# Optimization experiments

Measured on AMD Instinct MI355X. Metric: run time of the kernel, lower is better.

Reference implementation:

```python
import jax, jax.numpy as jnp
import numpy as np
from jax import lax

B, C_IN, L = 16, 2, 8192
D, H, NL = 256, 8, 4
DK = D // H
DFF = 2 * D
S = L // 8  # downsampled length = 1024
EPS = 1e-5


def _pe(seq, d):
    pos = jnp.arange(seq, dtype=jnp.float32)[:, None]
    div = jnp.exp(jnp.arange(0, d, 2, dtype=jnp.float32) * (-np.log(10000.0) / d))
    pe = jnp.zeros((seq, d), dtype=jnp.float32)
    pe = pe.at[:, 0::2].set(jnp.sin(pos * div))
    pe = pe.at[:, 1::2].set(jnp.cos(pos * div))
    return pe  # (seq, d)


def _layernorm(x, g, b):
    m = jnp.mean(x, axis=-1, keepdims=True)
    v = jnp.mean((x - m) ** 2, axis=-1, keepdims=True)
    return (x - m) * lax.rsqrt(v + EPS) * g + b


def setup_inputs() -> dict:
    key = jax.random.key(0)
    ks = jax.random.split(key, 20)
    sd = 0.02
    inp = {
        'x': jax.random.normal(ks[0], (B, C_IN, L), jnp.float32),
        'conv1_w': jax.random.normal(ks[1], (32, C_IN, 8), jnp.float32) * sd,
        'conv1_b': jnp.zeros((32,), jnp.float32),
        'conv2_w': jax.random.normal(ks[2], (D, 32, 4), jnp.float32) * sd,
        'conv2_b': jnp.zeros((D,), jnp.float32),
        'wq': jax.random.normal(ks[3], (NL, D, D), jnp.float32) * sd,
        'bq': jnp.zeros((NL, D), jnp.float32),
        'wk': jax.random.normal(ks[4], (NL, D, D), jnp.float32) * sd,
        'bk': jnp.zeros((NL, D), jnp.float32),
        'wv': jax.random.normal(ks[5], (NL, D, D), jnp.float32) * sd,
        'bv': jnp.zeros((NL, D), jnp.float32),
        'wo': jax.random.normal(ks[6], (NL, D, D), jnp.float32) * sd,
        'bo': jnp.zeros((NL, D), jnp.float32),
        'ln1_g': jnp.ones((NL, D), jnp.float32),
        'ln1_b': jnp.zeros((NL, D), jnp.float32),
        'ff_w1': jax.random.normal(ks[7], (NL, D, DFF), jnp.float32) * sd,
        'ff_b1': jnp.zeros((NL, DFF), jnp.float32),
        'ff_w2': jax.random.normal(ks[8], (NL, DFF, D), jnp.float32) * sd,
        'ff_b2': jnp.zeros((NL, D), jnp.float32),
        'ln2_g': jnp.ones((NL, D), jnp.float32),
        'ln2_b': jnp.zeros((NL, D), jnp.float32),
        'cls_w1': jax.random.normal(ks[9], (D, D // 2), jnp.float32) * sd,
        'cls_b1': jnp.zeros((D // 2,), jnp.float32),
        'cls_w2': jax.random.normal(ks[10], (D // 2, 1), jnp.float32) * sd,
        'cls_b2': jnp.zeros((1,), jnp.float32),
    }
    return inp


def reference(x, conv1_w, conv1_b, conv2_w, conv2_b,
              wq, bq, wk, bk, wv, bv, wo, bo,
              ln1_g, ln1_b, ff_w1, ff_b1, ff_w2, ff_b2, ln2_g, ln2_b,
              cls_w1, cls_b1, cls_w2, cls_b2):
    dn = ('NCH', 'OIH', 'NCH')
    # downsampler: conv(k8,s4,p2) -> relu -> conv(k4,s2,p1) -> relu
    h = lax.conv_general_dilated(x, conv1_w, (4,), [(2, 2)], dimension_numbers=dn)
    h = jax.nn.relu(h + conv1_b[None, :, None])
    h = lax.conv_general_dilated(h, conv2_w, (2,), [(1, 1)], dimension_numbers=dn)
    h = jax.nn.relu(h + conv2_b[None, :, None])
    h = h.transpose(0, 2, 1)  # (B, S, D)
    h = h + _pe(h.shape[1], D)[None]
    scale = 1.0 / np.sqrt(DK)
    for i in range(NL):
        # multi-head attention (explicit QK^T -> softmax -> V)
        q = (h @ wq[i] + bq[i]).reshape(B, S, H, DK)
        k = (h @ wk[i] + bk[i]).reshape(B, S, H, DK)
        v = (h @ wv[i] + bv[i]).reshape(B, S, H, DK)
        scores = jnp.einsum('bqhd,bkhd->bhqk', q, k) * scale
        attn = jax.nn.softmax(scores, axis=-1)
        ctx = jnp.einsum('bhqk,bkhd->bqhd', attn, v).reshape(B, S, D)
        h = _layernorm(h + ctx @ wo[i] + bo[i], ln1_g[i], ln1_b[i])
        ff = jax.nn.relu(h @ ff_w1[i] + ff_b1[i]) @ ff_w2[i] + ff_b2[i]
        h = _layernorm(h + ff, ln2_g[i], ln2_b[i])
    pooled = jnp.mean(h, axis=1)  # (B, D)
    logits = jax.nn.relu(pooled @ cls_w1 + cls_b1) @ cls_w2 + cls_b2
    return jax.nn.sigmoid(logits)  # (B, 1)
```

## Files before the change

kernel.cpp:

```cpp
#include <hip/hip_runtime.h>
#include <math.h>

typedef unsigned short u16;
typedef __attribute__((ext_vector_type(8))) short bf16x8;
typedef __attribute__((ext_vector_type(4))) float f32x4;
typedef __attribute__((ext_vector_type(16))) float f32x16;

#define B_ 16
#define L_ 8192
#define D_ 256
#define H_ 8
#define NL_ 4
#define DFF_ 512
#define S_ 1024
#define L1_ 2048
#define MROWS_ 16384

__device__ __forceinline__ u16 f2bf(float f) {
    unsigned u = __float_as_uint(f);
    unsigned r = (u + 0x7fffu + ((u >> 16) & 1u)) >> 16;
    return (u16)r;
}
__device__ __forceinline__ float fexp2(float x) {
    return __builtin_amdgcn_exp2f(x);
}
__device__ __forceinline__ unsigned cvtpk(float a, float b) {
    unsigned r;
    asm("v_cvt_pk_bf16_f32 %0, %1, %2" : "=v"(r) : "v"(a), "v"(b));
    return r;
}
__device__ __forceinline__ void pl32swap(unsigned& dst, unsigned& src) {
    asm volatile("v_permlane32_swap_b32 %0, %1" : "+v"(dst), "+v"(src));
}

typedef __attribute__((address_space(1))) const void gvoid;
typedef __attribute__((address_space(3))) void lvoid;
__device__ __forceinline__ void gll16(const void* g, void* l) {
    __builtin_amdgcn_global_load_lds((gvoid*)g, (lvoid*)l, 16, 0, 0);
}
__device__ __forceinline__ void stage64(const u16* src, int ld, u16* lds, int tid) {
    gll16(src + (size_t)(tid >> 2) * ld + (tid & 3) * 8, lds + (tid >> 6) * 512);
}

__global__ __launch_bounds__(256) void conv1_kernel(const float* __restrict__ x,
                                                    const float* __restrict__ w,
                                                    const float* __restrict__ bias,
                                                    float* __restrict__ out) {
    int idx = blockIdx.x * 256 + threadIdx.x;
    int t = idx & 2047;
    int o = (idx >> 11) & 31;
    int b = idx >> 16;
    float s = bias[o];
    int base = t * 4 - 2;
#pragma unroll
    for (int c = 0; c < 2; ++c) {
        const float* xr = x + ((size_t)(b * 2 + c)) * L_;
        const float* wr = w + (o * 2 + c) * 8;
#pragma unroll
        for (int j = 0; j < 8; ++j) {
            int p = base + j;
            if (p >= 0 && p < L_) s += xr[p] * wr[j];
        }
    }
    out[idx] = fmaxf(s, 0.f);
}

__global__ __launch_bounds__(256) void im2col2_kernel(const float* __restrict__ h1,
                                                      u16* __restrict__ A2) {
    int idx = blockIdx.x * 256 + threadIdx.x;
    int k = idx & 127, row = idx >> 7;
    int c = k >> 2, j = k & 3;
    int b = row >> 10, s = row & 1023;
    int p = s * 2 - 1 + j;
    float v = (p >= 0 && p < L1_) ? h1[((size_t)(b * 32 + c) << 11) + p] : 0.f;
    A2[idx] = f2bf(v);
}

__global__ __launch_bounds__(256) void pack_all(const float* __restrict__ wq,
                                                const float* __restrict__ wk,
                                                const float* __restrict__ wv,
                                                const float* __restrict__ wo,
                                                const float* __restrict__ ff_w1,
                                                const float* __restrict__ ff_w2,
                                                const float* __restrict__ conv2_w,
                                                const float* __restrict__ bq,
                                                const float* __restrict__ bk,
                                                const float* __restrict__ bv,
                                                u16* __restrict__ qkvT, u16* __restrict__ woT,
                                                u16* __restrict__ ff1T, u16* __restrict__ ff2T,
                                                u16* __restrict__ w2cT,
                                                float* __restrict__ pe, float* __restrict__ bqkv,
                                                float* __restrict__ pooled, float qscale) {
    int id = blockIdx.x * 256 + threadIdx.x;
    if (id < 786432) {
        int l = id / 196608, j = id % 196608;
        int row = j >> 8, k = j & 255;
        const float* src; float sc = 1.f; int n;
        if (row < 256) { src = wq; n = row; sc = qscale; }
        else if (row < 512) { src = wk; n = row - 256; }
        else { src = wv; n = row - 512; }
        qkvT[id] = f2bf(src[((size_t)l * 256 + k) * 256 + n] * sc);
        return;
    }
    id -= 786432;
    if (id < 262144) {
        int l = id >> 16, j = id & 65535;
        int n = j >> 8, k = j & 255;
        woT[id] = f2bf(wo[((size_t)l * 256 + k) * 256 + n]);
        return;
    }
    id -= 262144;
    if (id < 524288) {
        int l = id >> 17, j = id & 131071;
        int n = j >> 8, k = j & 255;
        ff1T[id] = f2bf(ff_w1[((size_t)l * 256 + k) * 512 + n]);
        return;
    }
    id -= 524288;
    if (id < 524288) {
        int l = id >> 17, j = id & 131071;
        int n = j >> 9, k = j & 511;
        ff2T[id] = f2bf(ff_w2[((size_t)l * 512 + k) * 256 + n]);
        return;
    }
    id -= 524288;
    if (id < 32768) { w2cT[id] = f2bf(conv2_w[id]); return; }
    id -= 32768;
    if (id < 262144) {
        int s = id >> 8, d = id & 255;
        int i2 = d & ~1;
        float div = expf((float)i2 * (-9.210340371976184f / 256.f));
        float arg = (float)s * div;
        pe[id] = (d & 1) ? cosf(arg) : sinf(arg);
        return;
    }
    id -= 262144;
    if (id < 3072) {
        int l = id / 768, n = id % 768;
        const float* src = (n < 256) ? bq : (n < 512) ? bk : bv;
        float sc = (n < 256) ? qscale : 1.f;
        bqkv[id] = src[l * 256 + (n & 255)] * sc;
        return;
    }
    id -= 3072;
    if (id < 4096) pooled[id] = 0.f;
}

template <int EP>
__global__ __launch_bounds__(256) void mfma_gemm128(const u16* __restrict__ A, int lda,
                                                    const u16* __restrict__ WT,
                                                    const float* __restrict__ bias,
                                                    const float* __restrict__ pe,
                                                    float* __restrict__ hout,
                                                    u16* __restrict__ outB,
                                                    u16* __restrict__ ktout,
                                                    u16* __restrict__ vtout,
                                                    int N, int K) {
    __shared__ u16 Alds[128 * 32];
    __shared__ u16 Blds[128 * 32];
    int tid = threadIdx.x;
    int lane = tid & 63, w = tid >> 6;
    int lo = lane & 15, hi = lane >> 4;
    int m0 = blockIdx.y * 128;
    int n0 = blockIdx.x * 128;
    int wm = (w >> 1) * 64, wn = (w & 1) * 64;
    f32x4 acc[4][4];
#pragma unroll
    for (int i = 0; i < 4; ++i)
#pragma unroll
        for (int j = 0; j < 4; ++j) acc[i][j] = (f32x4){0.f, 0.f, 0.f, 0.f};

    for (int k0 = 0; k0 < K; k0 += 32) {
        stage64(A + (size_t)m0 * lda + k0, lda, Alds, tid);
        stage64(A + (size_t)(m0 + 64) * lda + k0, lda, Alds + 2048, tid);
        stage64(WT + (size_t)n0 * K + k0, K, Blds, tid);
        stage64(WT + (size_t)(n0 + 64) * K + k0, K, Blds + 2048, tid);
        __syncthreads();
        bf16x8 af[4], bfr[4];
#pragma unroll
        for (int mf = 0; mf < 4; ++mf) af[mf] = *(bf16x8*)&Alds[(wm + mf * 16 + lo) * 32 + hi * 8];
#pragma unroll
        for (int nf = 0; nf < 4; ++nf) bfr[nf] = *(bf16x8*)&Blds[(wn + nf * 16 + lo) * 32 + hi * 8];
#pragma unroll
        for (int mf = 0; mf < 4; ++mf)
#pragma unroll
            for (int nf = 0; nf < 4; ++nf)
                acc[mf][nf] = __builtin_amdgcn_mfma_f32_16x16x32_bf16(af[mf], bfr[nf], acc[mf][nf], 0, 0, 0);
        __syncthreads();
    }
#pragma unroll
    for (int mf = 0; mf < 4; ++mf)
#pragma unroll
        for (int nf = 0; nf < 4; ++nf) {
            int col = n0 + wn + nf * 16 + lo;
            float bb = bias[col];
            int rowb = m0 + wm + mf * 16 + hi * 4;
            if (EP == 3 && col >= 512) {
                int dc = col - 512;
                int bhh = ((rowb >> 10) << 3) + (dc >> 5);
                int s = rowb & 1023;
                unsigned u0 = (unsigned)f2bf(acc[mf][nf][0] + bb) |
                              ((unsigned)f2bf(acc[mf][nf][1] + bb) << 16);
                unsigned u1 = (unsigned)f2bf(acc[mf][nf][2] + bb) |
                              ((unsigned)f2bf(acc[mf][nf][3] + bb) << 16);
                uint2 val = {u0, u1};
                *(uint2*)(vtout + (((size_t)bhh * 32 + (s >> 5)) * 32 + (dc & 31)) * 32 + (s & 31)) = val;
            } else if (EP == 3 && col >= 256) {
                int kc = col - 256;
                int bhh = ((rowb >> 10) << 3) + (kc >> 5);
                int s = rowb & 1023;
                u16* kt_base = ktout + (((size_t)bhh * 32 + (s >> 5)) * 32) * 32;
#pragma unroll
                for (int r = 0; r < 4; ++r)
                    kt_base[((s & 31) + r) * 32 + (kc & 31)] = f2bf(acc[mf][nf][r] + bb);
            } else {
#pragma unroll
                for (int r = 0; r < 4; ++r) {
                    float v = acc[mf][nf][r] + bb;
                    if (EP == 1 || EP == 2) v = fmaxf(v, 0.f);
                    if (EP == 2) {
                        v += pe[((rowb + r) & 1023) * 256 + col];
                        hout[(size_t)(rowb + r) * 256 + col] = v;
                        outB[(size_t)(rowb + r) * 256 + col] = f2bf(v);
                    } else if (EP == 3) {
                        outB[(size_t)(rowb + r) * 256 + col] = f2bf(v);
                    } else {
                        outB[(size_t)(rowb + r) * N + col] = f2bf(v);
                    }
                }
            }
        }
}

template <int LAST>
__global__ __launch_bounds__(256) void mfma_gemm_ln(const u16* __restrict__ A, int lda,
                                                    const u16* __restrict__ WT,
                                                    const float* __restrict__ bias,
                                                    const float* __restrict__ resid,
                                                    const float* __restrict__ g,
                                                    const float* __restrict__ b2,
                                                    float* __restrict__ hout,
                                                    u16* __restrict__ hbout,
                                                    float* __restrict__ pooled,
                                                    int K) {
    __shared__ u16 Alds[32 * 32];
    __shared__ u16 Blds[256 * 32];
    __shared__ float red1[32][4];
    __shared__ float red2[32][4];
    int tid = threadIdx.x;
    int lane = tid & 63, w = tid >> 6;
    int lo = lane & 15, hi = lane >> 4;
    int m0 = blockIdx.x * 32;
    int wn = w * 64;
    f32x4 acc[2][4];
#pragma unroll
    for (int i = 0; i < 2; ++i)
#pragma unroll
        for (int j = 0; j < 4; ++j) acc[i][j] = (f32x4){0.f, 0.f, 0.f, 0.f};

    for (int k0 = 0; k0 < K; k0 += 32) {
        if (tid < 128)
            gll16(A + (size_t)(m0 + (tid >> 2)) * lda + k0 + (tid & 3) * 8, Alds + (tid >> 6) * 512);
        stage64(WT + (size_t)0 * K + k0, K, Blds, tid);
        stage64(WT + (size_t)64 * K + k0, K, Blds + 2048, tid);
        stage64(WT + (size_t)128 * K + k0, K, Blds + 4096, tid);
        stage64(WT + (size_t)192 * K + k0, K, Blds + 6144, tid);
        __syncthreads();
        bf16x8 af[2], bfr[4];
#pragma unroll
        for (int mf = 0; mf < 2; ++mf) af[mf] = *(bf16x8*)&Alds[(mf * 16 + lo) * 32 + hi * 8];
#pragma unroll
        for (int nf = 0; nf < 4; ++nf) bfr[nf] = *(bf16x8*)&Blds[(wn + nf * 16 + lo) * 32 + hi * 8];
#pragma unroll
        for (int mf = 0; mf < 2; ++mf)
#pragma unroll
            for (int nf = 0; nf < 4; ++nf)
                acc[mf][nf] = __builtin_amdgcn_mfma_f32_16x16x32_bf16(af[mf], bfr[nf], acc[mf][nf], 0, 0, 0);
        __syncthreads();
    }

#pragma unroll
    for (int mf = 0; mf < 2; ++mf)
#pragma unroll
        for (int nf = 0; nf < 4; ++nf) {
            int col = wn + nf * 16 + lo;
            float bb = bias[col];
#pragma unroll
            for (int r = 0; r < 4; ++r) {
                int row = m0 + mf * 16 + hi * 4 + r;
                acc[mf][nf][r] += bb + resid[(size_t)row * 256 + col];
            }
        }
#pragma unroll
    for (int mf = 0; mf < 2; ++mf)
#pragma unroll
        for (int r = 0; r < 4; ++r) {
            float s1 = acc[mf][0][r] + acc[mf][1][r] + acc[mf][2][r] + acc[mf][3][r];
            float s2 = acc[mf][0][r] * acc[mf][0][r] + acc[mf][1][r] * acc[mf][1][r] +
                       acc[mf][2][r] * acc[mf][2][r] + acc[mf][3][r] * acc[mf][3][r];
#pragma unroll
            for (int off = 1; off < 16; off <<= 1) {
                s1 += __shfl_xor(s1, off);
                s2 += __shfl_xor(s2, off);
            }
            if (lo == 0) {
                red1[mf * 16 + hi * 4 + r][w] = s1;
                red2[mf * 16 + hi * 4 + r][w] = s2;
            }
        }
    __syncthreads();
    float colsum[4] = {0.f, 0.f, 0.f, 0.f};
#pragma unroll
    for (int mf = 0; mf < 2; ++mf)
#pragma unroll
        for (int r = 0; r < 4; ++r) {
            int rl = mf * 16 + hi * 4 + r;
            float mean = (red1[rl][0] + red1[rl][1] + red1[rl][2] + red1[rl][3]) * (1.f / 256.f);
            float e2 = (red2[rl][0] + red2[rl][1] + red2[rl][2] + red2[rl][3]) * (1.f / 256.f);
            float rs = rsqrtf(e2 - mean * mean + 1e-5f);
#pragma unroll
            for (int nf = 0; nf < 4; ++nf) {
                int col = wn + nf * 16 + lo;
                float o = (acc[mf][nf][r] - mean) * rs * g[col] + b2[col];
                if (LAST) {
                    colsum[nf] += o;
                } else {
                    hout[(size_t)(m0 + rl) * 256 + col] = o;
                    hbout[(size_t)(m0 + rl) * 256 + col] = f2bf(o);
                }
            }
        }
    if (LAST) {
        int b = m0 >> 10;
#pragma unroll
        for (int nf = 0; nf < 4; ++nf) {
            float cs = colsum[nf];
            cs += __shfl_xor(cs, 16);
            cs += __shfl_xor(cs, 32);
            if (hi == 0) atomicAdd(&pooled[b * 256 + wn + nf * 16 + lo], cs);
        }
    }
}

__global__ __launch_bounds__(256) void attn_mfma(u16* __restrict__ qbuf,
                                                 const u16* __restrict__ ktiles,
                                                 const u16* __restrict__ vtiles) {
    int tid = threadIdx.x;
    int lane = tid & 63, w = tid >> 6;
    int q = lane & 31, h = lane >> 5;
    int phys = blockIdx.x;
    int bid = (phys & 7) * 128 + (phys >> 3);
    int qt = bid & 7, hh = (bid >> 3) & 7, bb = bid >> 6;
    int q0 = qt * 128 + w * 32;
    size_t rowbase = (size_t)bb * S_;

    const u16* qrow = qbuf + (rowbase + q0 + q) * 256 + hh * 32;
    bf16x8 qf0 = *(const bf16x8*)(qrow + h * 8);
    bf16x8 qf1 = *(const bf16x8*)(qrow + 16 + h * 8);

    const u16* kb = ktiles + (size_t)(bb * 8 + hh) * 32768 + q * 32 + h * 8;
    const u16* vb = vtiles + (size_t)(bb * 8 + hh) * 32768 + q * 32 + h * 8;

    f32x16 O = {0.f, 0.f, 0.f, 0.f, 0.f, 0.f, 0.f, 0.f, 0.f, 0.f, 0.f, 0.f, 0.f, 0.f, 0.f, 0.f};
    float l = 0.f;

#define LOADT(d0, d1, d2, d3, t)                         \
    {                                                    \
        const u16* kr = kb + (t) * 1024;                 \
        d0 = *(const bf16x8*)kr;                         \
        d1 = *(const bf16x8*)(kr + 16);                  \
        const u16* vr = vb + (t) * 1024;                 \
        d2 = *(const bf16x8*)vr;                         \
        d3 = *(const bf16x8*)(vr + 16);                  \
    }

#define TILE_BODY(kf0_, kf1_, vf0_, vf1_)                                               \
    {                                                                                   \
        f32x16 S = {0.f, 0.f, 0.f, 0.f, 0.f, 0.f, 0.f, 0.f,                             \
                    0.f, 0.f, 0.f, 0.f, 0.f, 0.f, 0.f, 0.f};                            \
        S = __builtin_amdgcn_mfma_f32_32x32x16_bf16(kf0_, qf0, S, 0, 0, 0);             \
        S = __builtin_amdgcn_mfma_f32_32x32x16_bf16(kf1_, qf1, S, 0, 0, 0);             \
        _Pragma("unroll") for (int i = 0; i < 16; ++i) S[i] = fexp2(S[i]);              \
        float t0 = (S[0] + S[1]) + (S[2] + S[3]);                                       \
        float t1 = (S[4] + S[5]) + (S[6] + S[7]);                                       \
        float t2 = (S[8] + S[9]) + (S[10] + S[11]);                                     \
        float t3 = (S[12] + S[13]) + (S[14] + S[15]);                                   \
        float ls = (t0 + t1) + (t2 + t3);                                               \
        unsigned ua = __float_as_uint(ls), ub = ua;                                     \
        pl32swap(ua, ub);                                                               \
        l += __uint_as_float(ua) + __uint_as_float(ub);                                 \
        unsigned pk[8];                                                                 \
        _Pragma("unroll") for (int i = 0; i < 8; ++i) pk[i] = cvtpk(S[2 * i], S[2 * i + 1]); \
        pl32swap(pk[2], pk[0]);                                                         \
        pl32swap(pk[3], pk[1]);                                                         \
        pl32swap(pk[6], pk[4]);                                                         \
        pl32swap(pk[7], pk[5]);                                                         \
        uint4 t4 = {pk[0], pk[1], pk[2], pk[3]};                                        \
        uint4 t5 = {pk[4], pk[5], pk[6], pk[7]};                                        \
        bf16x8 pf0 = *(bf16x8*)&t4;                                                     \
        bf16x8 pf1 = *(bf16x8*)&t5;                                                     \
        O = __builtin_amdgcn_mfma_f32_32x32x16_bf16(vf0_, pf0, O, 0, 0, 0);             \
        O = __builtin_amdgcn_mfma_f32_32x32x16_bf16(vf1_, pf1, O, 0, 0, 0);             \
    }

    bf16x8 ka0, ka1, va0, va1, kb0, kb1, vb0, vb1;
    LOADT(ka0, ka1, va0, va1, 0);
    LOADT(kb0, kb1, vb0, vb1, 1);
    for (int kt = 0; kt < 32; kt += 2) {
        bf16x8 kc0 = ka0, kc1 = ka1, vc0 = va0, vc1 = va1;
        if (kt + 2 < 32) LOADT(kc0, kc1, vc0, vc1, kt + 2);
        TILE_BODY(ka0, ka1, va0, va1);
        bf16x8 kd0 = kb0, kd1 = kb1, vd0 = vb0, vd1 = vb1;
        if (kt + 3 < 32) LOADT(kd0, kd1, vd0, vd1, kt + 3);
        TILE_BODY(kb0, kb1, vb0, vb1);
        ka0 = kc0; ka1 = kc1; va0 = vc0; va1 = vc1;
        kb0 = kd0; kb1 = kd1; vb0 = vd0; vb1 = vd1;
    }
#undef LOADT
#undef TILE_BODY

    float inv = 1.f / l;
    u16* orow = qbuf + (rowbase + q0 + q) * 256 + hh * 32;
#pragma unroll
    for (int gg = 0; gg < 4; ++gg) {
        unsigned u0 = cvtpk(O[4 * gg] * inv, O[4 * gg + 1] * inv);
        unsigned u1 = cvtpk(O[4 * gg + 2] * inv, O[4 * gg + 3] * inv);
        uint2 val = {u0, u1};
        *(uint2*)(orow + gg * 8 + h * 4) = val;
    }
}

__global__ __launch_bounds__(256) void cls_kernel(const float* __restrict__ pooled,
                                                  const float* __restrict__ w1,
                                                  const float* __restrict__ b1,
                                                  const float* __restrict__ w2,
                                                  const float* __restrict__ b2,
                                                  float* __restrict__ out) {
    int b = blockIdx.x;
    int d = threadIdx.x;
    __shared__ float pl[256];
    __shared__ float hid[128];
    pl[d] = pooled[b * 256 + d] * (1.f / 1024.f);
    __syncthreads();
    if (d < 128) {
        float a = b1[d];
        for (int k = 0; k < 256; ++k) a += pl[k] * w1[k * 128 + d];
        hid[d] = fmaxf(a, 0.f);
    }
    __syncthreads();
    if (d == 0) {
        float a = b2[0];
        for (int k = 0; k < 128; ++k) a += hid[k] * w2[k];
        out[b] = 1.f / (1.f + expf(-a));
    }
}

extern "C" void kernel_launch(void* const* d_in, const int* in_sizes, int n_in,
                              void* d_out, int out_size, void* d_ws, size_t ws_size,
                              hipStream_t stream) {
    const float* x       = (const float*)d_in[0];
    const float* conv1_w = (const float*)d_in[1];
    const float* conv1_b = (const float*)d_in[2];
    const float* conv2_w = (const float*)d_in[3];
    const float* conv2_b = (const float*)d_in[4];
    const float* wq      = (const float*)d_in[5];
    const float* bq      = (const float*)d_in[6];
    const float* wk      = (const float*)d_in[7];
    const float* bk      = (const float*)d_in[8];
    const float* wv      = (const float*)d_in[9];
    const float* bv      = (const float*)d_in[10];
    const float* wo      = (const float*)d_in[11];
    const float* bo      = (const float*)d_in[12];
    const float* ln1_g   = (const float*)d_in[13];
    const float* ln1_b   = (const float*)d_in[14];
    const float* ff_w1   = (const float*)d_in[15];
    const float* ff_b1   = (const float*)d_in[16];
    const float* ff_w2   = (const float*)d_in[17];
    const float* ff_b2   = (const float*)d_in[18];
    const float* ln2_g   = (const float*)d_in[19];
    const float* ln2_b   = (const float*)d_in[20];
    const float* cls_w1  = (const float*)d_in[21];
    const float* cls_b1  = (const float*)d_in[22];
    const float* cls_w2  = (const float*)d_in[23];
    const float* cls_b2  = (const float*)d_in[24];

    char* wsb = (char*)d_ws;
    float* h    = (float*)wsb;
    u16*   hb   = (u16*)(wsb + ((size_t)16 << 20));
    u16*   qbuf = (u16*)(wsb + ((size_t)24 << 20));
    u16*   ktl  = (u16*)(wsb + ((size_t)32 << 20));
    u16*   vtl  = (u16*)(wsb + ((size_t)40 << 20));
    u16*   ffh  = (u16*)(wsb + ((size_t)32 << 20));
    u16*   A2   = (u16*)(wsb + ((size_t)32 << 20));
    float* h1   = (float*)(wsb + ((size_t)36 << 20));
    float* pe   = (float*)(wsb + ((size_t)48 << 20));
    char*  pkb  = wsb + ((size_t)49 << 20);
    u16*   qkvT = (u16*)pkb;
    u16*   woT  = qkvT + (size_t)4 * 768 * 256;
    u16*   ff1T = woT + (size_t)4 * 256 * 256;
    u16*   ff2T = ff1T + (size_t)4 * 512 * 256;
    u16*   w2cT = ff2T + (size_t)4 * 512 * 256;
    float* bqkv = (float*)(w2cT + 256 * 128);
    float* pooled = bqkv + 4 * 768;

    const float qscale = 0.17677669529663687f * 1.4426950408889634f;
    pack_all<<<9372, 256, 0, stream>>>(wq, wk, wv, wo, ff_w1, ff_w2, conv2_w, bq, bk, bv,
                                       qkvT, woT, ff1T, ff2T, w2cT, pe, bqkv, pooled, qscale);

    conv1_kernel<<<4096, 256, 0, stream>>>(x, conv1_w, conv1_b, h1);
    im2col2_kernel<<<8192, 256, 0, stream>>>(h1, A2);
    mfma_gemm128<2><<<dim3(2, 128), 256, 0, stream>>>(A2, 128, w2cT, conv2_b, pe, h, hb,
                                                      nullptr, nullptr, 256, 128);

    for (int l = 0; l < NL_; ++l) {
        const u16* qkvT_l = qkvT + (size_t)l * 768 * 256;
        const u16* woT_l  = woT + (size_t)l * 256 * 256;
        const u16* ff1T_l = ff1T + (size_t)l * 512 * 256;
        const u16* ff2T_l = ff2T + (size_t)l * 256 * 512;

        mfma_gemm128<3><<<dim3(6, 128), 256, 0, stream>>>(hb, 256, qkvT_l, bqkv + l * 768,
                                                          nullptr, nullptr, qbuf, ktl, vtl, 256, 256);
        attn_mfma<<<1024, 256, 0, stream>>>(qbuf, ktl, vtl);
        mfma_gemm_ln<0><<<512, 256, 0, stream>>>(qbuf, 256, woT_l, bo + l * 256, h,
                                                 ln1_g + l * 256, ln1_b + l * 256, h, hb, nullptr, 256);
        mfma_gemm128<1><<<dim3(4, 128), 256, 0, stream>>>(hb, 256, ff1T_l, ff_b1 + l * 512,
                                                          nullptr, nullptr, ffh, nullptr, nullptr, 512, 256);
        if (l < NL_ - 1) {
            mfma_gemm_ln<0><<<512, 256, 0, stream>>>(ffh, 512, ff2T_l, ff_b2 + l * 256, h,
                                                     ln2_g + l * 256, ln2_b + l * 256, h, hb, nullptr, 512);
        } else {
            mfma_gemm_ln<1><<<512, 256, 0, stream>>>(ffh, 512, ff2T_l, ff_b2 + l * 256, h,
                                                     ln2_g + l * 256, ln2_b + l * 256, h, hb, pooled, 512);
        }
    }

    cls_kernel<<<B_, 256, 0, stream>>>(pooled, cls_w1, cls_b1, cls_w2, cls_b2, (float*)d_out);
}
```

Measured before the change: 564.9 us.

## Stage K/V tiles through swizzled LDS in attention and fuse conv1 into im2col

The attention kernel no longer has each wave read K and V tiles straight from global memory into registers. All four waves now share one copy of each 32x32 tile, loaded into double-buffered LDS with global_load_lds and synchronised by a barrier every tile. The QKV GEMM epilogue writes the K/V tiles in an XOR-swizzled layout to match, which avoids LDS bank conflicts. Separately, conv1 is fused into the im2col kernel so the h1 intermediate is never written, at the cost of computing conv1 about twice per output because the stride-2 windows overlap.

```diff
diff --git a/kernel.cpp b/kernel.cpp
--- a/kernel.cpp
+++ b/kernel.cpp
@@ -32,6 +32,7 @@
 __device__ __forceinline__ void pl32swap(unsigned& dst, unsigned& src) {
     asm volatile("v_permlane32_swap_b32 %0, %1" : "+v"(dst), "+v"(src));
 }
+__device__ __forceinline__ int swz16(int b) { return b ^ ((b >> 3) & 0x18); }
 
 typedef __attribute__((address_space(1))) const void gvoid;
 typedef __attribute__((address_space(3))) void lvoid;
@@ -42,37 +43,31 @@
     gll16(src + (size_t)(tid >> 2) * ld + (tid & 3) * 8, lds + (tid >> 6) * 512);
 }
 
-__global__ __launch_bounds__(256) void conv1_kernel(const float* __restrict__ x,
-                                                    const float* __restrict__ w,
-                                                    const float* __restrict__ bias,
-                                                    float* __restrict__ out) {
-    int idx = blockIdx.x * 256 + threadIdx.x;
-    int t = idx & 2047;
-    int o = (idx >> 11) & 31;
-    int b = idx >> 16;
-    float s = bias[o];
-    int base = t * 4 - 2;
-#pragma unroll
-    for (int c = 0; c < 2; ++c) {
-        const float* xr = x + ((size_t)(b * 2 + c)) * L_;
-        const float* wr = w + (o * 2 + c) * 8;
-#pragma unroll
-        for (int j = 0; j < 8; ++j) {
-            int p = base + j;
-            if (p >= 0 && p < L_) s += xr[p] * wr[j];
-        }
-    }
-    out[idx] = fmaxf(s, 0.f);
-}
-
-__global__ __launch_bounds__(256) void im2col2_kernel(const float* __restrict__ h1,
-                                                      u16* __restrict__ A2) {
+__global__ __launch_bounds__(256) void conv1_im2col_kernel(const float* __restrict__ x,
+                                                           const float* __restrict__ w,
+                                                           const float* __restrict__ bias,
+                                                           u16* __restrict__ A2) {
     int idx = blockIdx.x * 256 + threadIdx.x;
     int k = idx & 127, row = idx >> 7;
     int c = k >> 2, j = k & 3;
     int b = row >> 10, s = row & 1023;
     int p = s * 2 - 1 + j;
-    float v = (p >= 0 && p < L1_) ? h1[((size_t)(b * 32 + c) << 11) + p] : 0.f;
+    float v = 0.f;
+    if (p >= 0 && p < L1_) {
+        float acc = bias[c];
+        int base = p * 4 - 2;
+#pragma unroll
+        for (int ci = 0; ci < 2; ++ci) {
+            const float* xr = x + ((size_t)(b * 2 + ci)) * L_;
+            const float* wr = w + (c * 2 + ci) * 8;
+#pragma unroll
+            for (int jj = 0; jj < 8; ++jj) {
+                int pos = base + jj;
+                if (pos >= 0 && pos < L_) acc += xr[pos] * wr[jj];
+            }
+        }
+        v = fmaxf(acc, 0.f);
+    }
     A2[idx] = f2bf(v);
 }
 
@@ -204,15 +199,17 @@
                 unsigned u1 = (unsigned)f2bf(acc[mf][nf][2] + bb) |
                               ((unsigned)f2bf(acc[mf][nf][3] + bb) << 16);
                 uint2 val = {u0, u1};
-                *(uint2*)(vtout + (((size_t)bhh * 32 + (s >> 5)) * 32 + (dc & 31)) * 32 + (s & 31)) = val;
+                char* tile = (char*)vtout + ((size_t)bhh * 32 + (s >> 5)) * 2048;
+                *(uint2*)(tile + swz16(((dc & 31) * 32 + (s & 31)) * 2)) = val;
             } else if (EP == 3 && col >= 256) {
                 int kc = col - 256;
                 int bhh = ((rowb >> 10) << 3) + (kc >> 5);
                 int s = rowb & 1023;
-                u16* kt_base = ktout + (((size_t)bhh * 32 + (s >> 5)) * 32) * 32;
+                char* tile = (char*)ktout + ((size_t)bhh * 32 + (s >> 5)) * 2048;
 #pragma unroll
                 for (int r = 0; r < 4; ++r)
-                    kt_base[((s & 31) + r) * 32 + (kc & 31)] = f2bf(acc[mf][nf][r] + bb);
+                    *(u16*)(tile + swz16((((s & 31) + r) * 32 + (kc & 31)) * 2)) =
+                        f2bf(acc[mf][nf][r] + bb);
             } else {
 #pragma unroll
                 for (int r = 0; r < 4; ++r) {
@@ -345,6 +342,7 @@
 __global__ __launch_bounds__(256) void attn_mfma(u16* __restrict__ qbuf,
                                                  const u16* __restrict__ ktiles,
                                                  const u16* __restrict__ vtiles) {
+    __shared__ char sbuf[2][4096];
     int tid = threadIdx.x;
     int lane = tid & 63, w = tid >> 6;
     int q = lane & 31, h = lane >> 5;
@@ -358,66 +356,61 @@
     bf16x8 qf0 = *(const bf16x8*)(qrow + h * 8);
     bf16x8 qf1 = *(const bf16x8*)(qrow + 16 + h * 8);
 
-    const u16* kb = ktiles + (size_t)(bb * 8 + hh) * 32768 + q * 32 + h * 8;
-    const u16* vb = vtiles + (size_t)(bb * 8 + hh) * 32768 + q * 32 + h * 8;
+    const char* kt_g = (const char*)(ktiles + (size_t)(bb * 8 + hh) * 32768);
+    const char* vt_g = (const char*)(vtiles + (size_t)(bb * 8 + hh) * 32768);
+    const char* src_base = (tid < 128 ? kt_g : vt_g) + (tid & 127) * 16;
+    char* dst_half = &sbuf[0][0] + (tid >> 6) * 1024;
+
+    int koff0 = swz16(q * 64 + h * 16);
+    int koff1 = swz16(q * 64 + 32 + h * 16);
 
     f32x16 O = {0.f, 0.f, 0.f, 0.f, 0.f, 0.f, 0.f, 0.f, 0.f, 0.f, 0.f, 0.f, 0.f, 0.f, 0.f, 0.f};
     float l = 0.f;
 
-#define LOADT(d0, d1, d2, d3, t)                         \
-    {                                                    \
-        const u16* kr = kb + (t) * 1024;                 \
-        d0 = *(const bf16x8*)kr;                         \
-        d1 = *(const bf16x8*)(kr + 16);                  \
-        const u16* vr = vb + (t) * 1024;                 \
-        d2 = *(const bf16x8*)vr;                         \
-        d3 = *(const bf16x8*)(vr + 16);                  \
-    }
-
-#define TILE_BODY(kf0_, kf1_, vf0_, vf1_)                                               \
-    {                                                                                   \
-        f32x16 S = {0.f, 0.f, 0.f, 0.f, 0.f, 0.f, 0.f, 0.f,                             \
-                    0.f, 0.f, 0.f, 0.f, 0.f, 0.f, 0.f, 0.f};                            \
-        S = __builtin_amdgcn_mfma_f32_32x32x16_bf16(kf0_, qf0, S, 0, 0, 0);             \
-        S = __builtin_amdgcn_mfma_f32_32x32x16_bf16(kf1_, qf1, S, 0, 0, 0);             \
-        _Pragma("unroll") for (int i = 0; i < 16; ++i) S[i] = fexp2(S[i]);              \
-        float t0 = (S[0] + S[1]) + (S[2] + S[3]);                                       \
-        float t1 = (S[4] + S[5]) + (S[6] + S[7]);                                       \
-        float t2 = (S[8] + S[9]) + (S[10] + S[11]);                                     \
-        float t3 = (S[12] + S[13]) + (S[14] + S[15]);                                   \
-        float ls = (t0 + t1) + (t2 + t3);                                               \
-        unsigned ua = __float_as_uint(ls), ub = ua;                                     \
-        pl32swap(ua, ub);                                                               \
-        l += __uint_as_float(ua) + __uint_as_float(ub);                                 \
-        unsigned pk[8];                                                                 \
-        _Pragma("unroll") for (int i = 0; i < 8; ++i) pk[i] = cvtpk(S[2 * i], S[2 * i + 1]); \
-        pl32swap(pk[2], pk[0]);                                                         \
-        pl32swap(pk[3], pk[1]);                                                         \
-        pl32swap(pk[6], pk[4]);                                                         \
-        pl32swap(pk[7], pk[5]);                                                         \
-        uint4 t4 = {pk[0], pk[1], pk[2], pk[3]};                                        \
-        uint4 t5 = {pk[4], pk[5], pk[6], pk[7]};                                        \
-        bf16x8 pf0 = *(bf16x8*)&t4;                                                     \
-        bf16x8 pf1 = *(bf16x8*)&t5;                                                     \
-        O = __builtin_amdgcn_mfma_f32_32x32x16_bf16(vf0_, pf0, O, 0, 0, 0);             \
-        O = __builtin_amdgcn_mfma_f32_32x32x16_bf16(vf1_, pf1, O, 0, 0, 0);             \
-    }
-
-    bf16x8 ka0, ka1, va0, va1, kb0, kb1, vb0, vb1;
-    LOADT(ka0, ka1, va0, va1, 0);
-    LOADT(kb0, kb1, vb0, vb1, 1);
-    for (int kt = 0; kt < 32; kt += 2) {
-        bf16x8 kc0 = ka0, kc1 = ka1, vc0 = va0, vc1 = va1;
-        if (kt + 2 < 32) LOADT(kc0, kc1, vc0, vc1, kt + 2);
-        TILE_BODY(ka0, ka1, va0, va1);
-        bf16x8 kd0 = kb0, kd1 = kb1, vd0 = vb0, vd1 = vb1;
-        if (kt + 3 < 32) LOADT(kd0, kd1, vd0, vd1, kt + 3);
-        TILE_BODY(kb0, kb1, vb0, vb1);
-        ka0 = kc0; ka1 = kc1; va0 = vc0; va1 = vc1;
-        kb0 = kd0; kb1 = kd1; vb0 = vd0; vb1 = vd1;
-    }
-#undef LOADT
-#undef TILE_BODY
+    gll16(src_base, dst_half);
+    __syncthreads();
+
+    int cur = 0;
+    for (int t = 0; t < 32; ++t) {
+        if (t + 1 < 32) gll16(src_base + (size_t)(t + 1) * 2048, dst_half + (cur ^ 1) * 4096);
+        const char* kl = &sbuf[cur][0];
+        bf16x8 kf0 = *(const bf16x8*)(kl + koff0);
+        bf16x8 kf1 = *(const bf16x8*)(kl + koff1);
+        bf16x8 vf0 = *(const bf16x8*)(kl + 2048 + koff0);
+        bf16x8 vf1 = *(const bf16x8*)(kl + 2048 + koff1);
+
+        f32x16 S = {0.f, 0.f, 0.f, 0.f, 0.f, 0.f, 0.f, 0.f,
+                    0.f, 0.f, 0.f, 0.f, 0.f, 0.f, 0.f, 0.f};
+        S = __builtin_amdgcn_mfma_f32_32x32x16_bf16(kf0, qf0, S, 0, 0, 0);
+        S = __builtin_amdgcn_mfma_f32_32x32x16_bf16(kf1, qf1, S, 0, 0, 0);
+#pragma unroll
+        for (int i = 0; i < 16; ++i) S[i] = fexp2(S[i]);
+        float t0 = (S[0] + S[1]) + (S[2] + S[3]);
+        float t1 = (S[4] + S[5]) + (S[6] + S[7]);
+        float t2 = (S[8] + S[9]) + (S[10] + S[11]);
+        float t3 = (S[12] + S[13]) + (S[14] + S[15]);
+        float ls = (t0 + t1) + (t2 + t3);
+        unsigned ua = __float_as_uint(ls), ub = ua;
+        pl32swap(ua, ub);
+        l += __uint_as_float(ua) + __uint_as_float(ub);
+
+        unsigned pk[8];
+#pragma unroll
+        for (int i = 0; i < 8; ++i) pk[i] = cvtpk(S[2 * i], S[2 * i + 1]);
+        pl32swap(pk[2], pk[0]);
+        pl32swap(pk[3], pk[1]);
+        pl32swap(pk[6], pk[4]);
+        pl32swap(pk[7], pk[5]);
+        uint4 t4 = {pk[0], pk[1], pk[2], pk[3]};
+        uint4 t5 = {pk[4], pk[5], pk[6], pk[7]};
+        bf16x8 pf0 = *(bf16x8*)&t4;
+        bf16x8 pf1 = *(bf16x8*)&t5;
+        O = __builtin_amdgcn_mfma_f32_32x32x16_bf16(vf0, pf0, O, 0, 0, 0);
+        O = __builtin_amdgcn_mfma_f32_32x32x16_bf16(vf1, pf1, O, 0, 0, 0);
+
+        __syncthreads();
+        cur ^= 1;
+    }
 
     float inv = 1.f / l;
     u16* orow = qbuf + (rowbase + q0 + q) * 256 + hh * 32;
@@ -492,7 +485,6 @@
     u16*   vtl  = (u16*)(wsb + ((size_t)40 << 20));
     u16*   ffh  = (u16*)(wsb + ((size_t)32 << 20));
     u16*   A2   = (u16*)(wsb + ((size_t)32 << 20));
-    float* h1   = (float*)(wsb + ((size_t)36 << 20));
     float* pe   = (float*)(wsb + ((size_t)48 << 20));
     char*  pkb  = wsb + ((size_t)49 << 20);
     u16*   qkvT = (u16*)pkb;
@@ -507,8 +499,7 @@
     pack_all<<<9372, 256, 0, stream>>>(wq, wk, wv, wo, ff_w1, ff_w2, conv2_w, bq, bk, bv,
                                        qkvT, woT, ff1T, ff2T, w2cT, pe, bqkv, pooled, qscale);
 
-    conv1_kernel<<<4096, 256, 0, stream>>>(x, conv1_w, conv1_b, h1);
-    im2col2_kernel<<<8192, 256, 0, stream>>>(h1, A2);
+    conv1_im2col_kernel<<<8192, 256, 0, stream>>>(x, conv1_w, conv1_b, A2);
     mfma_gemm128<2><<<dim3(2, 128), 256, 0, stream>>>(A2, 128, w2cT, conv2_b, pe, h, hb,
                                                       nullptr, nullptr, 256, 128);
 
```

Measured after the change: 652.0 us. +15.4%, slower.
